# Performance work log

Measured on AMD Instinct MI355X. Metric: run time of the kernel, lower is better.

## Reference

```python
import jax, jax.numpy as jnp
import numpy as np

N = 50000
E = 800000
IN_DIM = 128
HEADS = 4
OUT_DIM = 32
LEAKY_ALPHA = 0.4
BN_EPS = 1e-5


def setup_inputs() -> dict:
    key = jax.random.key(0)
    k_x, k_e, k_w, k_as, k_at = jax.random.split(key, 5)
    x = jax.random.normal(k_x, (N, IN_DIM), dtype=jnp.float32)
    edge_index = jax.random.randint(k_e, (2, E), 0, N, dtype=jnp.int32)
    # Linear weight stored as (in_dim, heads*out_dim) so that h = x @ W
    w_bound = 1.0 / np.sqrt(IN_DIM)
    W = jax.random.uniform(k_w, (IN_DIM, HEADS * OUT_DIM), dtype=jnp.float32,
                           minval=-w_bound, maxval=w_bound)
    # xavier_uniform with gain=1.414 on (heads, out_dim)
    xav = 1.414 * np.sqrt(6.0 / (HEADS + OUT_DIM))
    a_src = jax.random.uniform(k_as, (HEADS, OUT_DIM), dtype=jnp.float32, minval=-xav, maxval=xav)
    a_tgt = jax.random.uniform(k_at, (HEADS, OUT_DIM), dtype=jnp.float32, minval=-xav, maxval=xav)
    # BatchNorm affine params (fresh init: gamma=1, beta=0)
    gamma = jnp.ones((HEADS * OUT_DIM,), dtype=jnp.float32)
    beta = jnp.zeros((HEADS * OUT_DIM,), dtype=jnp.float32)
    return {"x": x, "W": W, "a_src": a_src, "a_tgt": a_tgt,
            "gamma": gamma, "beta": beta, "edge_index": edge_index}


def reference(x, W, a_src, a_tgt, gamma, beta, edge_index):
    src = edge_index[0]
    tgt = edge_index[1]
    n = x.shape[0]
    # Linear projection -> (N, H, D)
    h = (x @ W).reshape(n, HEADS, OUT_DIM)
    h_src = h[src]   # (E, H, D)
    h_tgt = h[tgt]   # (E, H, D)
    # Per-edge, per-head attention logits
    e_src = jnp.einsum('ehd,hd->eh', h_src, a_src)
    e_tgt = jnp.einsum('ehd,hd->eh', h_tgt, a_tgt)
    e = jax.nn.leaky_relu(e_src + e_tgt, negative_slope=LEAKY_ALPHA)
    # Global (per-head) max subtraction for numerical stability, as in original
    e = e - jnp.max(e, axis=0, keepdims=True)
    alpha = jnp.exp(e)  # (E, H)
    # Segment softmax denominator over target nodes
    alpha_sum = jax.ops.segment_sum(alpha, tgt, num_segments=n) + 1e-16  # (N, H)
    alpha = alpha / alpha_sum[tgt]
    # dropout is identity in eval mode
    # Weighted aggregation of source features into targets
    h_prime = h_src * alpha[:, :, None]  # (E, H, D)
    out = jax.ops.segment_sum(h_prime, tgt, num_segments=n)  # (N, H, D)
    out = out.reshape(n, HEADS * OUT_DIM)  # concat=True
    # BatchNorm1d in training mode: biased batch statistics
    mean = jnp.mean(out, axis=0)
    var = jnp.mean(jnp.square(out - mean), axis=0)
    out = (out - mean) * jax.lax.rsqrt(var + BN_EPS) * gamma + beta
    return out
```

## Files before the change

kernel.cpp:

```cpp
#include <hip/hip_runtime.h>
#include <math.h>

#define N_NODES 50000
#define E_EDGES 800000
#define IN_DIM 128
#define HEADS 4
#define OUT_DIM 32
#define HD 128
#define LEAKY 0.4f
#define BN_EPS 1e-5f

#define BSH 7
#define NB ((N_NODES + 127) >> BSH)
#define FB 196
#define FCH 4096
#define PCAP 2560
#define SRTCAP 3072
#define SCCH ((NB + 63) / 64)

typedef __attribute__((ext_vector_type(8))) short short8;
typedef __attribute__((ext_vector_type(8))) unsigned short us8;
typedef __attribute__((ext_vector_type(4))) float f32x4;

__device__ __forceinline__ unsigned enc_max(float f) {
    unsigned u = __float_as_uint(f);
    return ((int)u >= 0) ? (u | 0x80000000u) : ~u;
}
__device__ __forceinline__ float dec_max(unsigned u) {
    return (u & 0x80000000u) ? __uint_as_float(u ^ 0x80000000u)
                             : __uint_as_float(~u);
}

__device__ __forceinline__ float leaky(float v) {
    return v > 0.f ? v : LEAKY * v;
}

__device__ __forceinline__ unsigned short f2bf(float f) {
    unsigned u = __float_as_uint(f);
    u = (u + 0x7FFFu + ((u >> 16) & 1u)) >> 16;
    return (unsigned short)u;
}
__device__ __forceinline__ float bf2f(unsigned short u) {
    return __uint_as_float(((unsigned)u) << 16);
}

__global__ __launch_bounds__(256) void kb_fill(
    const int* __restrict__ src, const int* __restrict__ tgt,
    int* __restrict__ bcur, int* __restrict__ ebkt,
    const float* __restrict__ W, unsigned short* __restrict__ wswz)
{
    if (blockIdx.x >= FB) {
        int base = (blockIdx.x - FB) * 1024;
        for (int idx = base + threadIdx.x; idx < base + 1024; idx += 256) {
            int l  = idx & 63;
            int f  = idx >> 6;
            int nt = f >> 2, kc = f & 3;
            int kbase = kc * 32 + ((l >> 4) << 3);
            int col   = nt * 16 + (l & 15);
            unsigned short* dst = &wswz[idx * 8];
#pragma unroll
            for (int j = 0; j < 8; j++)
                dst[j] = f2bf(W[(kbase + j) * HD + col]);
        }
        return;
    }
    __shared__ int hist[NB];
    __shared__ int rbase[NB];
    int beg = blockIdx.x * FCH;
    int end = min(beg + FCH, E_EDGES);
    for (int i = threadIdx.x; i < NB; i += 256) hist[i] = 0;
    __syncthreads();
    for (int e = beg + threadIdx.x; e < end; e += 256)
        atomicAdd(&hist[tgt[e] >> BSH], 1);
    __syncthreads();
    for (int i = threadIdx.x; i < NB; i += 256) {
        int c = hist[i];
        if (c) {
            int r = atomicAdd(&bcur[i], c);
            rbase[i] = i * PCAP + min(r, PCAP);
        }
    }
    __syncthreads();
    for (int i = threadIdx.x; i < NB; i += 256) hist[i] = 0;
    __syncthreads();
    for (int e = beg + threadIdx.x; e < end; e += 256) {
        int tv = tgt[e], b = tv >> BSH;
        int off = atomicAdd(&hist[b], 1);
        int idx = rbase[b] + off;
        if (idx < (b + 1) * PCAP)
            ebkt[idx] = src[e] | ((tv & 127) << 16);
    }
}

__global__ __launch_bounds__(256) void kb_sort(
    const int* __restrict__ bcur, const int* __restrict__ ebkt,
    int* __restrict__ rowptr, unsigned short* __restrict__ esrc)
{
    __shared__ int ebl[SRTCAP];
    __shared__ int srt[SRTCAP];
    __shared__ int csc[NB + 1];
    __shared__ int bins[128];
    __shared__ int deg_l[128], excl_l[128], cur_l[128];
    __shared__ int wtot, btot;
    int b    = blockIdx.x;
    int tid  = threadIdx.x;
    int lane = tid & 63, wv = tid >> 6;

    for (int i = tid; i < NB; i += 256) csc[i] = min(bcur[i], PCAP);
    if (tid < 128) { deg_l[tid] = 0; cur_l[tid] = 0; bins[tid] = 0; }
    __syncthreads();
    if (tid < 64) {
        int cb = tid * SCCH;
        int loc[SCCH];
        int sum = 0;
#pragma unroll
        for (int k = 0; k < SCCH; k++) {
            int idx = cb + k;
            int v = (idx < NB) ? csc[idx] : 0;
            loc[k] = sum; sum += v;
        }
        int ss = sum;
#pragma unroll
        for (int off = 1; off < 64; off <<= 1) {
            int u = __shfl_up(ss, off, 64);
            if (tid >= off) ss += u;
        }
        int excl = ss - sum;
#pragma unroll
        for (int k = 0; k < SCCH; k++) {
            int idx = cb + k;
            if (idx < NB) csc[idx] = excl + loc[k];
        }
        if (tid == 63) {
            csc[NB] = excl + sum;
            if (b == 0) rowptr[N_NODES] = excl + sum;
        }
    }
    __syncthreads();
    int base_in = b * PCAP;
    int base    = csc[b];
    int cnt     = csc[b + 1] - base;

    for (int j = tid; j < cnt; j += 256) {
        int p = ebkt[base_in + j];
        ebl[j] = p;
        atomicAdd(&bins[(p & 0xFFFF) >> 9], 1);
    }
    __syncthreads();
    {
        int v = (tid < 128) ? bins[tid] : 0;
        int s = v;
#pragma unroll
        for (int off = 1; off < 64; off <<= 1) {
            int u = __shfl_up(s, off, 64);
            if (lane >= off) s += u;
        }
        if (tid == 63) btot = s;
        __syncthreads();
        if (tid < 128) bins[tid] = s - v + ((wv == 1) ? btot : 0);
        __syncthreads();
    }
    for (int j = tid; j < cnt; j += 256) {
        int p = ebl[j];
        int pos = atomicAdd(&bins[(p & 0xFFFF) >> 9], 1);
        srt[pos] = p;
    }
    __syncthreads();
    for (int j = tid; j < cnt; j += 256)
        atomicAdd(&deg_l[srt[j] >> 16], 1);
    __syncthreads();

    int v = (tid < 128) ? deg_l[tid] : 0;
    int s = v;
#pragma unroll
    for (int off = 1; off < 64; off <<= 1) {
        int u = __shfl_up(s, off, 64);
        if (lane >= off) s += u;
    }
    if (tid == 63) wtot = s;
    __syncthreads();
    if (tid < 128) {
        int ex = s - v + ((wv == 1) ? wtot : 0);
        excl_l[tid] = ex;
        int node = (b << BSH) + tid;
        if (node < N_NODES) rowptr[node] = base + ex;
    }
    __syncthreads();
    for (int j = tid; j < cnt; j += 256) {
        int p  = srt[j];
        int tl = p >> 16;
        int off = atomicAdd(&cur_l[tl], 1);
        esrc[base + excl_l[tl] + off] = (unsigned short)(p & 0xFFFF);
    }
}

__global__ __launch_bounds__(256) void k1_mfma(
    const float* __restrict__ x, const unsigned short* __restrict__ wswz,
    const float* __restrict__ a_src, const float* __restrict__ a_tgt,
    unsigned short* __restrict__ hb, float* __restrict__ s,
    float* __restrict__ t)
{
    __shared__ __align__(16) unsigned short Wl[32 * 64 * 8];
    const int tid = threadIdx.x;
    for (int idx = tid; idx < 2048; idx += 256)
        ((us8*)Wl)[idx] = ((const us8*)wswz)[idx];
    __syncthreads();

    const int wave = tid >> 6, lane = tid & 63;
    const int quad = lane >> 4, rl = lane & 15;
    const int row0 = blockIdx.x * 64 + wave * 16;
    const int crow = min(row0 + rl, N_NODES - 1);

    short8 a[4];
    const float* xp = x + (size_t)crow * IN_DIM + quad * 8;
#pragma unroll
    for (int kc = 0; kc < 4; kc++) {
        float4 v0 = *(const float4*)(xp + kc * 32);
        float4 v1 = *(const float4*)(xp + kc * 32 + 4);
        short8 av;
        av[0] = (short)f2bf(v0.x); av[1] = (short)f2bf(v0.y);
        av[2] = (short)f2bf(v0.z); av[3] = (short)f2bf(v0.w);
        av[4] = (short)f2bf(v1.x); av[5] = (short)f2bf(v1.y);
        av[6] = (short)f2bf(v1.z); av[7] = (short)f2bf(v1.w);
        a[kc] = av;
    }

    float asv[8], atv[8];
#pragma unroll
    for (int nt = 0; nt < 8; nt++) {
        asv[nt] = a_src[nt * 16 + rl];
        atv[nt] = a_tgt[nt * 16 + rl];
    }

    float ps[4][4], pt[4][4];
#pragma unroll
    for (int hh = 0; hh < 4; hh++)
#pragma unroll
        for (int r = 0; r < 4; r++) { ps[hh][r] = 0.f; pt[hh][r] = 0.f; }

#pragma unroll
    for (int nt = 0; nt < 8; nt++) {
        f32x4 acc = {0.f, 0.f, 0.f, 0.f};
#pragma unroll
        for (int kc = 0; kc < 4; kc++) {
            short8 b = *(const short8*)&Wl[((nt * 4 + kc) * 64 + lane) * 8];
            acc = __builtin_amdgcn_mfma_f32_16x16x32_bf16(a[kc], b, acc, 0, 0, 0);
        }
        const int ocol = nt * 16 + rl;
        const int hh   = nt >> 1;
#pragma unroll
        for (int r = 0; r < 4; r++) {
            int orow = row0 + quad * 4 + r;
            if (orow < N_NODES)
                hb[(size_t)orow * HD + ocol] = f2bf(acc[r]);
            ps[hh][r] = fmaf(acc[r], asv[nt], ps[hh][r]);
            pt[hh][r] = fmaf(acc[r], atv[nt], pt[hh][r]);
        }
    }

#pragma unroll
    for (int m = 1; m <= 8; m <<= 1) {
#pragma unroll
        for (int hh = 0; hh < 4; hh++)
#pragma unroll
            for (int r = 0; r < 4; r++) {
                ps[hh][r] += __shfl_xor(ps[hh][r], m, 64);
                pt[hh][r] += __shfl_xor(pt[hh][r], m, 64);
            }
    }
    if (rl == 0) {
#pragma unroll
        for (int r = 0; r < 4; r++) {
            int orow = row0 + quad * 4 + r;
            if (orow < N_NODES) {
#pragma unroll
                for (int hh = 0; hh < 4; hh++) {
                    s[orow * HEADS + hh] = ps[hh][r];
                    t[orow * HEADS + hh] = pt[hh][r];
                }
            }
        }
    }
}

#define K2_BLOCKS 32
__global__ __launch_bounds__(256) void k2_nodemax(
    const float* __restrict__ s, const float* __restrict__ t,
    unsigned* __restrict__ smax, unsigned* __restrict__ tmax)
{
    float sm0 = -INFINITY, sm1 = -INFINITY, sm2 = -INFINITY, sm3 = -INFINITY;
    float tm0 = -INFINITY, tm1 = -INFINITY, tm2 = -INFINITY, tm3 = -INFINITY;
    for (int n = blockIdx.x * 256 + threadIdx.x; n < N_NODES;
         n += K2_BLOCKS * 256) {
        float4 s4 = ((const float4*)s)[n];
        float4 t4 = ((const float4*)t)[n];
        sm0 = fmaxf(sm0, s4.x); sm1 = fmaxf(sm1, s4.y);
        sm2 = fmaxf(sm2, s4.z); sm3 = fmaxf(sm3, s4.w);
        tm0 = fmaxf(tm0, t4.x); tm1 = fmaxf(tm1, t4.y);
        tm2 = fmaxf(tm2, t4.z); tm3 = fmaxf(tm3, t4.w);
    }
#pragma unroll
    for (int m = 32; m >= 1; m >>= 1) {
        sm0 = fmaxf(sm0, __shfl_xor(sm0, m, 64));
        sm1 = fmaxf(sm1, __shfl_xor(sm1, m, 64));
        sm2 = fmaxf(sm2, __shfl_xor(sm2, m, 64));
        sm3 = fmaxf(sm3, __shfl_xor(sm3, m, 64));
        tm0 = fmaxf(tm0, __shfl_xor(tm0, m, 64));
        tm1 = fmaxf(tm1, __shfl_xor(tm1, m, 64));
        tm2 = fmaxf(tm2, __shfl_xor(tm2, m, 64));
        tm3 = fmaxf(tm3, __shfl_xor(tm3, m, 64));
    }
    __shared__ float red[4][8];
    int wid = threadIdx.x >> 6;
    if ((threadIdx.x & 63) == 0) {
        red[wid][0] = sm0; red[wid][1] = sm1; red[wid][2] = sm2; red[wid][3] = sm3;
        red[wid][4] = tm0; red[wid][5] = tm1; red[wid][6] = tm2; red[wid][7] = tm3;
    }
    __syncthreads();
    if (threadIdx.x < 8) {
        float v = fmaxf(fmaxf(red[0][threadIdx.x], red[1][threadIdx.x]),
                        fmaxf(red[2][threadIdx.x], red[3][threadIdx.x]));
        unsigned* dst = (threadIdx.x < 4) ? &smax[threadIdx.x]
                                          : &tmax[threadIdx.x - 4];
        atomicMax(dst, enc_max(v));
    }
}

__global__ __launch_bounds__(256) void k4_pull(
    const int* __restrict__ rowptr, const unsigned short* __restrict__ esrc,
    const float* __restrict__ s, const float* __restrict__ t,
    const unsigned* __restrict__ smax, const unsigned* __restrict__ tmax,
    const unsigned short* __restrict__ hb, unsigned short* __restrict__ outpb)
{
    int g = blockIdx.x * 256 + threadIdx.x;
    int node = g >> 4;
    int lane = g & 15;
    if (node >= N_NODES) return;
    int head = lane >> 2;
    int beg = rowptr[node];
    int end = rowptr[node + 1];
    float mx = leaky(dec_max(smax[head]) + dec_max(tmax[head]));
    float tv = t[node * HEADS + head];

    float p0 = 0.f, p1 = 0.f, p2 = 0.f, p3 = 0.f;
    float p4 = 0.f, p5 = 0.f, p6 = 0.f, p7 = 0.f, psum = 0.f;
    float q0 = 0.f, q1 = 0.f, q2 = 0.f, q3 = 0.f;
    float q4 = 0.f, q5 = 0.f, q6 = 0.f, q7 = 0.f, qsum = 0.f;
    const unsigned short* hbase = hb + lane * 8;

    for (int j = beg; j < end; j += 8) {
        int lim = end - j;
        int si[8];
#pragma unroll
        for (int u = 0; u < 8; u++) {
            int uu = (u < lim) ? u : (lim - 1);
            si[u] = esrc[j + uu];
        }
        float sv[8];
        us8 hv[8];
#pragma unroll
        for (int u = 0; u < 8; u++) {
            sv[u] = s[si[u] * HEADS + head];
            hv[u] = *(const us8*)(hbase + (size_t)si[u] * HD);
        }
        float al[8];
#pragma unroll
        for (int u = 0; u < 8; u++) {
            float a = __expf(leaky(sv[u] + tv) - mx);
            al[u] = (u < lim) ? a : 0.f;
        }
#pragma unroll
        for (int u = 0; u < 8; u += 2) {
            float a0 = al[u], a1 = al[u + 1];
            p0 = fmaf(a0, bf2f(hv[u][0]), p0);  q0 = fmaf(a1, bf2f(hv[u+1][0]), q0);
            p1 = fmaf(a0, bf2f(hv[u][1]), p1);  q1 = fmaf(a1, bf2f(hv[u+1][1]), q1);
            p2 = fmaf(a0, bf2f(hv[u][2]), p2);  q2 = fmaf(a1, bf2f(hv[u+1][2]), q2);
            p3 = fmaf(a0, bf2f(hv[u][3]), p3);  q3 = fmaf(a1, bf2f(hv[u+1][3]), q3);
            p4 = fmaf(a0, bf2f(hv[u][4]), p4);  q4 = fmaf(a1, bf2f(hv[u+1][4]), q4);
            p5 = fmaf(a0, bf2f(hv[u][5]), p5);  q5 = fmaf(a1, bf2f(hv[u+1][5]), q5);
            p6 = fmaf(a0, bf2f(hv[u][6]), p6);  q6 = fmaf(a1, bf2f(hv[u+1][6]), q6);
            p7 = fmaf(a0, bf2f(hv[u][7]), p7);  q7 = fmaf(a1, bf2f(hv[u+1][7]), q7);
            psum += a0; qsum += a1;
        }
    }

    float w = 1.0f / (psum + qsum + 1e-16f);
    us8 o;
    o[0] = f2bf((p0 + q0) * w); o[1] = f2bf((p1 + q1) * w);
    o[2] = f2bf((p2 + q2) * w); o[3] = f2bf((p3 + q3) * w);
    o[4] = f2bf((p4 + q4) * w); o[5] = f2bf((p5 + q5) * w);
    o[6] = f2bf((p6 + q6) * w); o[7] = f2bf((p7 + q7) * w);
    *(us8*)(outpb + (size_t)node * HD + lane * 8) = o;
}

__global__ __launch_bounds__(256) void k5_stats(
    const unsigned short* __restrict__ outpb,
    float* __restrict__ bnsum, float* __restrict__ bnsq)
{
    __shared__ float lsum[HD], lsq[HD];
    int c8  = threadIdx.x & 15;
    int grp = threadIdx.x >> 4;
    if (threadIdx.x < HD) { lsum[threadIdx.x] = 0.f; lsq[threadIdx.x] = 0.f; }
    __syncthreads();
    int base = blockIdx.x * 256;
    int end  = min(base + 256, N_NODES);
    float sm[8], sq[8];
#pragma unroll
    for (int i = 0; i < 8; i++) { sm[i] = 0.f; sq[i] = 0.f; }
    for (int r = base + grp; r < end; r += 16) {
        us8 v = *(const us8*)(outpb + (size_t)r * HD + c8 * 8);
#pragma unroll
        for (int i = 0; i < 8; i++) {
            float f = bf2f(v[i]);
            sm[i] += f;
            sq[i] = fmaf(f, f, sq[i]);
        }
    }
#pragma unroll
    for (int i = 0; i < 8; i++) {
        atomicAdd(&lsum[c8 * 8 + i], sm[i]);
        atomicAdd(&lsq[c8 * 8 + i], sq[i]);
    }
    __syncthreads();
    if (threadIdx.x < HD) {
        unsafeAtomicAdd(&bnsum[threadIdx.x], lsum[threadIdx.x]);
        unsafeAtomicAdd(&bnsq[threadIdx.x], lsq[threadIdx.x]);
    }
}

__global__ __launch_bounds__(256) void k6_apply(
    const unsigned short* __restrict__ outpb,
    const float* __restrict__ bnsum, const float* __restrict__ bnsq,
    const float* __restrict__ gamma, const float* __restrict__ beta,
    float* __restrict__ out)
{
    int c8  = threadIdx.x & 15;
    int grp = threadIdx.x >> 4;
    int base = blockIdx.x * 256;
    int end  = min(base + 256, N_NODES);
    float inv_n = 1.0f / (float)N_NODES;
    float scale[8], shift[8];
#pragma unroll
    for (int i = 0; i < 8; i++) {
        int c = c8 * 8 + i;
        float mean = bnsum[c] * inv_n;
        float var  = bnsq[c] * inv_n - mean * mean;
        float sc   = gamma[c] * rsqrtf(var + BN_EPS);
        scale[i] = sc;
        shift[i] = beta[c] - mean * sc;
    }
    for (int r = base + grp; r < end; r += 16) {
        us8 v = *(const us8*)(outpb + (size_t)r * HD + c8 * 8);
        float4 o0, o1;
        o0.x = fmaf(bf2f(v[0]), scale[0], shift[0]);
        o0.y = fmaf(bf2f(v[1]), scale[1], shift[1]);
        o0.z = fmaf(bf2f(v[2]), scale[2], shift[2]);
        o0.w = fmaf(bf2f(v[3]), scale[3], shift[3]);
        o1.x = fmaf(bf2f(v[4]), scale[4], shift[4]);
        o1.y = fmaf(bf2f(v[5]), scale[5], shift[5]);
        o1.z = fmaf(bf2f(v[6]), scale[6], shift[6]);
        o1.w = fmaf(bf2f(v[7]), scale[7], shift[7]);
        float* op = out + (size_t)r * HD + c8 * 8;
        ((float4*)op)[0] = o0;
        ((float4*)op)[1] = o1;
    }
}

extern "C" void kernel_launch(void* const* d_in, const int* in_sizes, int n_in,
                              void* d_out, int out_size, void* d_ws, size_t ws_size,
                              hipStream_t stream)
{
    const float* x     = (const float*)d_in[0];
    const float* W     = (const float*)d_in[1];
    const float* a_src = (const float*)d_in[2];
    const float* a_tgt = (const float*)d_in[3];
    const float* gamma = (const float*)d_in[4];
    const float* beta  = (const float*)d_in[5];
    const int*   eidx  = (const int*)d_in[6];
    const int* src = eidx;
    const int* tgt = eidx + E_EDGES;
    float* out = (float*)d_out;

    unsigned short* hb    = (unsigned short*)d_ws;
    float*          s     = (float*)d_ws + 3200000;
    float*          t     = s + (size_t)N_NODES * HEADS;
    unsigned short* outpb = (unsigned short*)(t + (size_t)N_NODES * HEADS);
    int*            ebkt  = (int*)outpb;
    unsigned short* esrc  = outpb + 6400000;
    int*            rowptr= (int*)(esrc + E_EDGES);
    int*      bcur  = rowptr + N_NODES + 1;
    unsigned* smax  = (unsigned*)(bcur + 392);
    unsigned* tmax  = smax + 4;
    float*    bnsum = (float*)(tmax + 4);
    float*    bnsq  = bnsum + HD;
    size_t zero_bytes = (392 + 8 + HD + HD) * 4;
    hipMemsetAsync(bcur, 0, zero_bytes, stream);
    unsigned short* wswz = (unsigned short*)(((uintptr_t)(bnsq + HD) + 63) &
                                             ~(uintptr_t)63);

    kb_fill<<<FB + 2, 256, 0, stream>>>(src, tgt, bcur, ebkt, W, wswz);
    kb_sort<<<NB, 256, 0, stream>>>(bcur, ebkt, rowptr, esrc);

    k1_mfma<<<(N_NODES + 63) / 64, 256, 0, stream>>>(x, wswz, a_src, a_tgt,
                                                     hb, s, t);
    k2_nodemax<<<K2_BLOCKS, 256, 0, stream>>>(s, t, smax, tmax);
    long long k4_threads = (long long)N_NODES * 16;
    k4_pull<<<(unsigned)((k4_threads + 255) / 256), 256, 0, stream>>>(
        rowptr, esrc, s, t, smax, tmax, hb, outpb);
    k5_stats<<<(N_NODES + 255) / 256, 256, 0, stream>>>(outpb, bnsum, bnsq);
    k6_apply<<<(N_NODES + 255) / 256, 256, 0, stream>>>(outpb, bnsum, bnsq,
                                                        gamma, beta, out);
}
```

Baseline: 195.7 us.

## Merge pipeline into four kernels: gemm+bucket fill, sort+max, pull+stats, apply

Cuts the launch chain from seven kernels to four. Independent work now shares a launch: the projection GEMM runs alongside edge bucketing, with each GEMM block converting W to bf16 itself, and the CSR sort runs alongside the per-head max reduction. BatchNorm statistics are accumulated inside the pull-aggregation kernel instead of a separate pass that re-reads the output, and the sums are spread over 32 partial slots to reduce global atomic contention. The trade-offs are that every GEMM block now redoes the W conversion, and per-element shared atomics are added to the pull kernel.

```diff
diff --git a/kernel.cpp b/kernel.cpp
--- a/kernel.cpp
+++ b/kernel.cpp
@@ -17,6 +17,9 @@
 #define PCAP 2560
 #define SRTCAP 3072
 #define SCCH ((NB + 63) / 64)
+#define K1B ((N_NODES + 63) / 64)
+#define K2_BLOCKS 32
+#define NPART 32
 
 typedef __attribute__((ext_vector_type(8))) short short8;
 typedef __attribute__((ext_vector_type(8))) unsigned short us8;
@@ -44,166 +47,68 @@
     return __uint_as_float(((unsigned)u) << 16);
 }
 
-__global__ __launch_bounds__(256) void kb_fill(
+struct FillSh { int est[FCH]; int hist[NB]; int rbase[NB]; };
+union F1Sh { unsigned short Wl[32 * 64 * 8]; FillSh fl; };
+
+__global__ __launch_bounds__(256) void f1_gemm_fill(
+    const float* __restrict__ x, const float* __restrict__ W,
+    const float* __restrict__ a_src, const float* __restrict__ a_tgt,
     const int* __restrict__ src, const int* __restrict__ tgt,
     int* __restrict__ bcur, int* __restrict__ ebkt,
-    const float* __restrict__ W, unsigned short* __restrict__ wswz)
-{
-    if (blockIdx.x >= FB) {
-        int base = (blockIdx.x - FB) * 1024;
-        for (int idx = base + threadIdx.x; idx < base + 1024; idx += 256) {
-            int l  = idx & 63;
-            int f  = idx >> 6;
-            int nt = f >> 2, kc = f & 3;
-            int kbase = kc * 32 + ((l >> 4) << 3);
-            int col   = nt * 16 + (l & 15);
-            unsigned short* dst = &wswz[idx * 8];
-#pragma unroll
-            for (int j = 0; j < 8; j++)
-                dst[j] = f2bf(W[(kbase + j) * HD + col]);
-        }
-        return;
-    }
-    __shared__ int hist[NB];
-    __shared__ int rbase[NB];
-    int beg = blockIdx.x * FCH;
-    int end = min(beg + FCH, E_EDGES);
-    for (int i = threadIdx.x; i < NB; i += 256) hist[i] = 0;
-    __syncthreads();
-    for (int e = beg + threadIdx.x; e < end; e += 256)
-        atomicAdd(&hist[tgt[e] >> BSH], 1);
-    __syncthreads();
-    for (int i = threadIdx.x; i < NB; i += 256) {
-        int c = hist[i];
-        if (c) {
-            int r = atomicAdd(&bcur[i], c);
-            rbase[i] = i * PCAP + min(r, PCAP);
-        }
-    }
-    __syncthreads();
-    for (int i = threadIdx.x; i < NB; i += 256) hist[i] = 0;
-    __syncthreads();
-    for (int e = beg + threadIdx.x; e < end; e += 256) {
-        int tv = tgt[e], b = tv >> BSH;
-        int off = atomicAdd(&hist[b], 1);
-        int idx = rbase[b] + off;
-        if (idx < (b + 1) * PCAP)
-            ebkt[idx] = src[e] | ((tv & 127) << 16);
-    }
-}
-
-__global__ __launch_bounds__(256) void kb_sort(
-    const int* __restrict__ bcur, const int* __restrict__ ebkt,
-    int* __restrict__ rowptr, unsigned short* __restrict__ esrc)
-{
-    __shared__ int ebl[SRTCAP];
-    __shared__ int srt[SRTCAP];
-    __shared__ int csc[NB + 1];
-    __shared__ int bins[128];
-    __shared__ int deg_l[128], excl_l[128], cur_l[128];
-    __shared__ int wtot, btot;
-    int b    = blockIdx.x;
-    int tid  = threadIdx.x;
-    int lane = tid & 63, wv = tid >> 6;
-
-    for (int i = tid; i < NB; i += 256) csc[i] = min(bcur[i], PCAP);
-    if (tid < 128) { deg_l[tid] = 0; cur_l[tid] = 0; bins[tid] = 0; }
-    __syncthreads();
-    if (tid < 64) {
-        int cb = tid * SCCH;
-        int loc[SCCH];
-        int sum = 0;
-#pragma unroll
-        for (int k = 0; k < SCCH; k++) {
-            int idx = cb + k;
-            int v = (idx < NB) ? csc[idx] : 0;
-            loc[k] = sum; sum += v;
-        }
-        int ss = sum;
-#pragma unroll
-        for (int off = 1; off < 64; off <<= 1) {
-            int u = __shfl_up(ss, off, 64);
-            if (tid >= off) ss += u;
-        }
-        int excl = ss - sum;
-#pragma unroll
-        for (int k = 0; k < SCCH; k++) {
-            int idx = cb + k;
-            if (idx < NB) csc[idx] = excl + loc[k];
-        }
-        if (tid == 63) {
-            csc[NB] = excl + sum;
-            if (b == 0) rowptr[N_NODES] = excl + sum;
-        }
-    }
-    __syncthreads();
-    int base_in = b * PCAP;
-    int base    = csc[b];
-    int cnt     = csc[b + 1] - base;
-
-    for (int j = tid; j < cnt; j += 256) {
-        int p = ebkt[base_in + j];
-        ebl[j] = p;
-        atomicAdd(&bins[(p & 0xFFFF) >> 9], 1);
-    }
-    __syncthreads();
-    {
-        int v = (tid < 128) ? bins[tid] : 0;
-        int s = v;
-#pragma unroll
-        for (int off = 1; off < 64; off <<= 1) {
-            int u = __shfl_up(s, off, 64);
-            if (lane >= off) s += u;
-        }
-        if (tid == 63) btot = s;
-        __syncthreads();
-        if (tid < 128) bins[tid] = s - v + ((wv == 1) ? btot : 0);
-        __syncthreads();
-    }
-    for (int j = tid; j < cnt; j += 256) {
-        int p = ebl[j];
-        int pos = atomicAdd(&bins[(p & 0xFFFF) >> 9], 1);
-        srt[pos] = p;
-    }
-    __syncthreads();
-    for (int j = tid; j < cnt; j += 256)
-        atomicAdd(&deg_l[srt[j] >> 16], 1);
-    __syncthreads();
-
-    int v = (tid < 128) ? deg_l[tid] : 0;
-    int s = v;
-#pragma unroll
-    for (int off = 1; off < 64; off <<= 1) {
-        int u = __shfl_up(s, off, 64);
-        if (lane >= off) s += u;
-    }
-    if (tid == 63) wtot = s;
-    __syncthreads();
-    if (tid < 128) {
-        int ex = s - v + ((wv == 1) ? wtot : 0);
-        excl_l[tid] = ex;
-        int node = (b << BSH) + tid;
-        if (node < N_NODES) rowptr[node] = base + ex;
-    }
-    __syncthreads();
-    for (int j = tid; j < cnt; j += 256) {
-        int p  = srt[j];
-        int tl = p >> 16;
-        int off = atomicAdd(&cur_l[tl], 1);
-        esrc[base + excl_l[tl] + off] = (unsigned short)(p & 0xFFFF);
-    }
-}
-
-__global__ __launch_bounds__(256) void k1_mfma(
-    const float* __restrict__ x, const unsigned short* __restrict__ wswz,
-    const float* __restrict__ a_src, const float* __restrict__ a_tgt,
     unsigned short* __restrict__ hb, float* __restrict__ s,
     float* __restrict__ t)
 {
-    __shared__ __align__(16) unsigned short Wl[32 * 64 * 8];
+    __shared__ F1Sh sh;
     const int tid = threadIdx.x;
-    for (int idx = tid; idx < 2048; idx += 256)
-        ((us8*)Wl)[idx] = ((const us8*)wswz)[idx];
+
+    if (blockIdx.x >= K1B) {
+        int* est   = sh.fl.est;
+        int* hist  = sh.fl.hist;
+        int* rbase = sh.fl.rbase;
+        int beg = (blockIdx.x - K1B) * FCH;
+        int cnt = min(beg + FCH, E_EDGES) - beg;
+        for (int i = tid; i < NB; i += 256) hist[i] = 0;
+        __syncthreads();
+        for (int j = tid; j < cnt; j += 256) {
+            int sv = src[beg + j], tv = tgt[beg + j];
+            est[j] = sv | (tv << 16);
+            atomicAdd(&hist[tv >> BSH], 1);
+        }
+        __syncthreads();
+        for (int i = tid; i < NB; i += 256) {
+            int c = hist[i];
+            if (c) {
+                int r = atomicAdd(&bcur[i], c);
+                rbase[i] = i * PCAP + min(r, PCAP);
+            }
+        }
+        __syncthreads();
+        for (int i = tid; i < NB; i += 256) hist[i] = 0;
+        __syncthreads();
+        for (int j = tid; j < cnt; j += 256) {
+            int p  = est[j];
+            int tv = (int)((unsigned)p >> 16);
+            int b  = tv >> BSH;
+            int off = atomicAdd(&hist[b], 1);
+            int idx = rbase[b] + off;
+            if (idx < (b + 1) * PCAP)
+                ebkt[idx] = (p & 0xFFFF) | ((tv & 127) << 16);
+        }
+        return;
+    }
+
+    unsigned short* Wl = sh.Wl;
+    for (int idx = tid; idx < 2048; idx += 256) {
+        int l  = idx & 63;
+        int f  = idx >> 6;
+        int nt = f >> 2, kc = f & 3;
+        int kbase = kc * 32 + ((l >> 4) << 3);
+        int col   = nt * 16 + (l & 15);
+        unsigned short* dst = &Wl[idx * 8];
+#pragma unroll
+        for (int j = 0; j < 8; j++)
+            dst[j] = f2bf(W[(kbase + j) * HD + col]);
+    }
     __syncthreads();
 
     const int wave = tid >> 6, lane = tid & 63;
@@ -283,59 +188,174 @@
     }
 }
 
-#define K2_BLOCKS 32
-__global__ __launch_bounds__(256) void k2_nodemax(
+struct SortSh {
+    int ebl[SRTCAP]; int srt[SRTCAP]; int csc[NB + 1];
+    int bins[128]; int deg_l[128]; int excl_l[128]; int cur_l[128];
+    int wtot; int btot;
+};
+union F2Sh { SortSh so; float red[4][8]; };
+
+__global__ __launch_bounds__(256) void f2_sort_max(
+    const int* __restrict__ bcur, const int* __restrict__ ebkt,
+    int* __restrict__ rowptr, unsigned short* __restrict__ esrc,
     const float* __restrict__ s, const float* __restrict__ t,
     unsigned* __restrict__ smax, unsigned* __restrict__ tmax)
 {
-    float sm0 = -INFINITY, sm1 = -INFINITY, sm2 = -INFINITY, sm3 = -INFINITY;
-    float tm0 = -INFINITY, tm1 = -INFINITY, tm2 = -INFINITY, tm3 = -INFINITY;
-    for (int n = blockIdx.x * 256 + threadIdx.x; n < N_NODES;
-         n += K2_BLOCKS * 256) {
-        float4 s4 = ((const float4*)s)[n];
-        float4 t4 = ((const float4*)t)[n];
-        sm0 = fmaxf(sm0, s4.x); sm1 = fmaxf(sm1, s4.y);
-        sm2 = fmaxf(sm2, s4.z); sm3 = fmaxf(sm3, s4.w);
-        tm0 = fmaxf(tm0, t4.x); tm1 = fmaxf(tm1, t4.y);
-        tm2 = fmaxf(tm2, t4.z); tm3 = fmaxf(tm3, t4.w);
-    }
-#pragma unroll
-    for (int m = 32; m >= 1; m >>= 1) {
-        sm0 = fmaxf(sm0, __shfl_xor(sm0, m, 64));
-        sm1 = fmaxf(sm1, __shfl_xor(sm1, m, 64));
-        sm2 = fmaxf(sm2, __shfl_xor(sm2, m, 64));
-        sm3 = fmaxf(sm3, __shfl_xor(sm3, m, 64));
-        tm0 = fmaxf(tm0, __shfl_xor(tm0, m, 64));
-        tm1 = fmaxf(tm1, __shfl_xor(tm1, m, 64));
-        tm2 = fmaxf(tm2, __shfl_xor(tm2, m, 64));
-        tm3 = fmaxf(tm3, __shfl_xor(tm3, m, 64));
-    }
-    __shared__ float red[4][8];
-    int wid = threadIdx.x >> 6;
-    if ((threadIdx.x & 63) == 0) {
-        red[wid][0] = sm0; red[wid][1] = sm1; red[wid][2] = sm2; red[wid][3] = sm3;
-        red[wid][4] = tm0; red[wid][5] = tm1; red[wid][6] = tm2; red[wid][7] = tm3;
-    }
-    __syncthreads();
-    if (threadIdx.x < 8) {
-        float v = fmaxf(fmaxf(red[0][threadIdx.x], red[1][threadIdx.x]),
-                        fmaxf(red[2][threadIdx.x], red[3][threadIdx.x]));
-        unsigned* dst = (threadIdx.x < 4) ? &smax[threadIdx.x]
-                                          : &tmax[threadIdx.x - 4];
-        atomicMax(dst, enc_max(v));
-    }
-}
-
-__global__ __launch_bounds__(256) void k4_pull(
+    __shared__ F2Sh sh;
+    int tid  = threadIdx.x;
+    int lane = tid & 63, wv = tid >> 6;
+
+    if (blockIdx.x >= NB) {
+        int bI = blockIdx.x - NB;
+        float sm0 = -INFINITY, sm1 = -INFINITY, sm2 = -INFINITY, sm3 = -INFINITY;
+        float tm0 = -INFINITY, tm1 = -INFINITY, tm2 = -INFINITY, tm3 = -INFINITY;
+        for (int n = bI * 256 + tid; n < N_NODES; n += K2_BLOCKS * 256) {
+            float4 s4 = ((const float4*)s)[n];
+            float4 t4 = ((const float4*)t)[n];
+            sm0 = fmaxf(sm0, s4.x); sm1 = fmaxf(sm1, s4.y);
+            sm2 = fmaxf(sm2, s4.z); sm3 = fmaxf(sm3, s4.w);
+            tm0 = fmaxf(tm0, t4.x); tm1 = fmaxf(tm1, t4.y);
+            tm2 = fmaxf(tm2, t4.z); tm3 = fmaxf(tm3, t4.w);
+        }
+#pragma unroll
+        for (int m = 32; m >= 1; m >>= 1) {
+            sm0 = fmaxf(sm0, __shfl_xor(sm0, m, 64));
+            sm1 = fmaxf(sm1, __shfl_xor(sm1, m, 64));
+            sm2 = fmaxf(sm2, __shfl_xor(sm2, m, 64));
+            sm3 = fmaxf(sm3, __shfl_xor(sm3, m, 64));
+            tm0 = fmaxf(tm0, __shfl_xor(tm0, m, 64));
+            tm1 = fmaxf(tm1, __shfl_xor(tm1, m, 64));
+            tm2 = fmaxf(tm2, __shfl_xor(tm2, m, 64));
+            tm3 = fmaxf(tm3, __shfl_xor(tm3, m, 64));
+        }
+        if (lane == 0) {
+            sh.red[wv][0] = sm0; sh.red[wv][1] = sm1;
+            sh.red[wv][2] = sm2; sh.red[wv][3] = sm3;
+            sh.red[wv][4] = tm0; sh.red[wv][5] = tm1;
+            sh.red[wv][6] = tm2; sh.red[wv][7] = tm3;
+        }
+        __syncthreads();
+        if (tid < 8) {
+            float v = fmaxf(fmaxf(sh.red[0][tid], sh.red[1][tid]),
+                            fmaxf(sh.red[2][tid], sh.red[3][tid]));
+            unsigned* dst = (tid < 4) ? &smax[tid] : &tmax[tid - 4];
+            atomicMax(dst, enc_max(v));
+        }
+        return;
+    }
+
+    int b = blockIdx.x;
+    int* ebl    = sh.so.ebl;
+    int* srt    = sh.so.srt;
+    int* csc    = sh.so.csc;
+    int* bins   = sh.so.bins;
+    int* deg_l  = sh.so.deg_l;
+    int* excl_l = sh.so.excl_l;
+    int* cur_l  = sh.so.cur_l;
+
+    for (int i = tid; i < NB; i += 256) csc[i] = min(bcur[i], PCAP);
+    if (tid < 128) { deg_l[tid] = 0; cur_l[tid] = 0; bins[tid] = 0; }
+    __syncthreads();
+    if (tid < 64) {
+        int cb = tid * SCCH;
+        int loc[SCCH];
+        int sum = 0;
+#pragma unroll
+        for (int k = 0; k < SCCH; k++) {
+            int idx = cb + k;
+            int v = (idx < NB) ? csc[idx] : 0;
+            loc[k] = sum; sum += v;
+        }
+        int ss = sum;
+#pragma unroll
+        for (int off = 1; off < 64; off <<= 1) {
+            int u = __shfl_up(ss, off, 64);
+            if (tid >= off) ss += u;
+        }
+        int excl = ss - sum;
+#pragma unroll
+        for (int k = 0; k < SCCH; k++) {
+            int idx = cb + k;
+            if (idx < NB) csc[idx] = excl + loc[k];
+        }
+        if (tid == 63) {
+            csc[NB] = excl + sum;
+            if (b == 0) rowptr[N_NODES] = excl + sum;
+        }
+    }
+    __syncthreads();
+    int base_in = b * PCAP;
+    int base    = csc[b];
+    int cnt     = csc[b + 1] - base;
+
+    for (int j = tid; j < cnt; j += 256) {
+        int p = ebkt[base_in + j];
+        ebl[j] = p;
+        atomicAdd(&bins[(p & 0xFFFF) >> 9], 1);
+    }
+    __syncthreads();
+    {
+        int v = (tid < 128) ? bins[tid] : 0;
+        int ssv = v;
+#pragma unroll
+        for (int off = 1; off < 64; off <<= 1) {
+            int u = __shfl_up(ssv, off, 64);
+            if (lane >= off) ssv += u;
+        }
+        if (tid == 63) sh.so.btot = ssv;
+        __syncthreads();
+        if (tid < 128) bins[tid] = ssv - v + ((wv == 1) ? sh.so.btot : 0);
+        __syncthreads();
+    }
+    for (int j = tid; j < cnt; j += 256) {
+        int p = ebl[j];
+        int pos = atomicAdd(&bins[(p & 0xFFFF) >> 9], 1);
+        srt[pos] = p;
+    }
+    __syncthreads();
+    for (int j = tid; j < cnt; j += 256)
+        atomicAdd(&deg_l[srt[j] >> 16], 1);
+    __syncthreads();
+
+    int v = (tid < 128) ? deg_l[tid] : 0;
+    int sv2 = v;
+#pragma unroll
+    for (int off = 1; off < 64; off <<= 1) {
+        int u = __shfl_up(sv2, off, 64);
+        if (lane >= off) sv2 += u;
+    }
+    if (tid == 63) sh.so.wtot = sv2;
+    __syncthreads();
+    if (tid < 128) {
+        int ex = sv2 - v + ((wv == 1) ? sh.so.wtot : 0);
+        excl_l[tid] = ex;
+        int node = (b << BSH) + tid;
+        if (node < N_NODES) rowptr[node] = base + ex;
+    }
+    __syncthreads();
+    for (int j = tid; j < cnt; j += 256) {
+        int p  = srt[j];
+        int tl = p >> 16;
+        int off = atomicAdd(&cur_l[tl], 1);
+        esrc[base + excl_l[tl] + off] = (unsigned short)(p & 0xFFFF);
+    }
+}
+
+__global__ __launch_bounds__(256) void f3_pull_stats(
     const int* __restrict__ rowptr, const unsigned short* __restrict__ esrc,
     const float* __restrict__ s, const float* __restrict__ t,
     const unsigned* __restrict__ smax, const unsigned* __restrict__ tmax,
-    const unsigned short* __restrict__ hb, unsigned short* __restrict__ outpb)
+    const unsigned short* __restrict__ hb, unsigned short* __restrict__ outpb,
+    float* __restrict__ bnsum_part, float* __restrict__ bnsq_part)
 {
-    int g = blockIdx.x * 256 + threadIdx.x;
+    __shared__ float lsum[HD], lsq[HD];
+    int tid = threadIdx.x;
+    if (tid < HD) { lsum[tid] = 0.f; lsq[tid] = 0.f; }
+    __syncthreads();
+
+    int g = blockIdx.x * 256 + tid;
     int node = g >> 4;
     int lane = g & 15;
-    if (node >= N_NODES) return;
     int head = lane >> 2;
     int beg = rowptr[node];
     int end = rowptr[node + 1];
@@ -391,64 +411,55 @@
     o[4] = f2bf((p4 + q4) * w); o[5] = f2bf((p5 + q5) * w);
     o[6] = f2bf((p6 + q6) * w); o[7] = f2bf((p7 + q7) * w);
     *(us8*)(outpb + (size_t)node * HD + lane * 8) = o;
-}
-
-__global__ __launch_bounds__(256) void k5_stats(
+
+#pragma unroll
+    for (int i = 0; i < 8; i++) {
+        float f = bf2f(o[i]);
+        atomicAdd(&lsum[lane * 8 + i], f);
+        atomicAdd(&lsq[lane * 8 + i], f * f);
+    }
+    __syncthreads();
+    if (tid < HD) {
+        int ps = blockIdx.x & (NPART - 1);
+        unsafeAtomicAdd(&bnsum_part[ps * HD + tid], lsum[tid]);
+        unsafeAtomicAdd(&bnsq_part [ps * HD + tid], lsq[tid]);
+    }
+}
+
+__global__ __launch_bounds__(256) void f4_apply(
     const unsigned short* __restrict__ outpb,
-    float* __restrict__ bnsum, float* __restrict__ bnsq)
-{
-    __shared__ float lsum[HD], lsq[HD];
-    int c8  = threadIdx.x & 15;
-    int grp = threadIdx.x >> 4;
-    if (threadIdx.x < HD) { lsum[threadIdx.x] = 0.f; lsq[threadIdx.x] = 0.f; }
-    __syncthreads();
-    int base = blockIdx.x * 256;
-    int end  = min(base + 256, N_NODES);
-    float sm[8], sq[8];
-#pragma unroll
-    for (int i = 0; i < 8; i++) { sm[i] = 0.f; sq[i] = 0.f; }
-    for (int r = base + grp; r < end; r += 16) {
-        us8 v = *(const us8*)(outpb + (size_t)r * HD + c8 * 8);
-#pragma unroll
-        for (int i = 0; i < 8; i++) {
-            float f = bf2f(v[i]);
-            sm[i] += f;
-            sq[i] = fmaf(f, f, sq[i]);
-        }
-    }
-#pragma unroll
-    for (int i = 0; i < 8; i++) {
-        atomicAdd(&lsum[c8 * 8 + i], sm[i]);
-        atomicAdd(&lsq[c8 * 8 + i], sq[i]);
-    }
-    __syncthreads();
-    if (threadIdx.x < HD) {
-        unsafeAtomicAdd(&bnsum[threadIdx.x], lsum[threadIdx.x]);
-        unsafeAtomicAdd(&bnsq[threadIdx.x], lsq[threadIdx.x]);
-    }
-}
-
-__global__ __launch_bounds__(256) void k6_apply(
-    const unsigned short* __restrict__ outpb,
-    const float* __restrict__ bnsum, const float* __restrict__ bnsq,
+    const float* __restrict__ bnsum_part, const float* __restrict__ bnsq_part,
     const float* __restrict__ gamma, const float* __restrict__ beta,
     float* __restrict__ out)
 {
-    int c8  = threadIdx.x & 15;
-    int grp = threadIdx.x >> 4;
+    __shared__ float scs[HD], shs[HD];
+    int tid = threadIdx.x;
+    if (tid < HD) {
+        float sm = 0.f, sq = 0.f;
+#pragma unroll 4
+        for (int p = 0; p < NPART; p++) {
+            sm += bnsum_part[p * HD + tid];
+            sq += bnsq_part [p * HD + tid];
+        }
+        float inv_n = 1.0f / (float)N_NODES;
+        float mean = sm * inv_n;
+        float var  = sq * inv_n - mean * mean;
+        float sc   = gamma[tid] * rsqrtf(var + BN_EPS);
+        scs[tid] = sc;
+        shs[tid] = beta[tid] - mean * sc;
+    }
+    __syncthreads();
+
+    int c8  = tid & 15;
+    int grp = tid >> 4;
+    float scale[8], shift[8];
+#pragma unroll
+    for (int i = 0; i < 8; i++) {
+        scale[i] = scs[c8 * 8 + i];
+        shift[i] = shs[c8 * 8 + i];
+    }
     int base = blockIdx.x * 256;
     int end  = min(base + 256, N_NODES);
-    float inv_n = 1.0f / (float)N_NODES;
-    float scale[8], shift[8];
-#pragma unroll
-    for (int i = 0; i < 8; i++) {
-        int c = c8 * 8 + i;
-        float mean = bnsum[c] * inv_n;
-        float var  = bnsq[c] * inv_n - mean * mean;
-        float sc   = gamma[c] * rsqrtf(var + BN_EPS);
-        scale[i] = sc;
-        shift[i] = beta[c] - mean * sc;
-    }
     for (int r = base + grp; r < end; r += 16) {
         us8 v = *(const us8*)(outpb + (size_t)r * HD + c8 * 8);
         float4 o0, o1;
@@ -491,23 +502,18 @@
     int*      bcur  = rowptr + N_NODES + 1;
     unsigned* smax  = (unsigned*)(bcur + 392);
     unsigned* tmax  = smax + 4;
-    float*    bnsum = (float*)(tmax + 4);
-    float*    bnsq  = bnsum + HD;
-    size_t zero_bytes = (392 + 8 + HD + HD) * 4;
+    float*    bnsum_part = (float*)(tmax + 4);
+    float*    bnsq_part  = bnsum_part + NPART * HD;
+    size_t zero_bytes = (392 + 8 + 2 * NPART * HD) * 4;
     hipMemsetAsync(bcur, 0, zero_bytes, stream);
-    unsigned short* wswz = (unsigned short*)(((uintptr_t)(bnsq + HD) + 63) &
-                                             ~(uintptr_t)63);
-
-    kb_fill<<<FB + 2, 256, 0, stream>>>(src, tgt, bcur, ebkt, W, wswz);
-    kb_sort<<<NB, 256, 0, stream>>>(bcur, ebkt, rowptr, esrc);
-
-    k1_mfma<<<(N_NODES + 63) / 64, 256, 0, stream>>>(x, wswz, a_src, a_tgt,
-                                                     hb, s, t);
-    k2_nodemax<<<K2_BLOCKS, 256, 0, stream>>>(s, t, smax, tmax);
-    long long k4_threads = (long long)N_NODES * 16;
-    k4_pull<<<(unsigned)((k4_threads + 255) / 256), 256, 0, stream>>>(
-        rowptr, esrc, s, t, smax, tmax, hb, outpb);
-    k5_stats<<<(N_NODES + 255) / 256, 256, 0, stream>>>(outpb, bnsum, bnsq);
-    k6_apply<<<(N_NODES + 255) / 256, 256, 0, stream>>>(outpb, bnsum, bnsq,
-                                                        gamma, beta, out);
-}
+
+    f1_gemm_fill<<<K1B + FB, 256, 0, stream>>>(x, W, a_src, a_tgt,
+                                               src, tgt, bcur, ebkt,
+                                               hb, s, t);
+    f2_sort_max<<<NB + K2_BLOCKS, 256, 0, stream>>>(bcur, ebkt, rowptr, esrc,
+                                                    s, t, smax, tmax);
+    f3_pull_stats<<<(N_NODES * 16) / 256, 256, 0, stream>>>(
+        rowptr, esrc, s, t, smax, tmax, hb, outpb, bnsum_part, bnsq_part);
+    f4_apply<<<(N_NODES + 255) / 256, 256, 0, stream>>>(
+        outpb, bnsum_part, bnsq_part, gamma, beta, out);
+}
```

After: 219.9 us. +12.4%, slower.
